# Kernel tuning notes

Measured on AMD Instinct MI355X. Metric: run time of the kernel, lower is better.

## Reference

```python
import jax, jax.numpy as jnp
import numpy as np

B, T, D, H = 8, 1024, 512, 8
HD = D // H
EPS = 1e-5


def setup_inputs() -> dict:
    key = jax.random.key(0)
    ks = jax.random.split(key, 16)
    s = 0.02
    return {
        "query": jax.random.normal(ks[0], (B, T, D), jnp.float32),
        "key": jax.random.normal(ks[1], (B, T, D), jnp.float32),
        "value": jax.random.normal(ks[2], (B, T, D), jnp.float32),
        "frac": jax.random.uniform(ks[3], (B, T), jnp.float32),
        "Wq": jax.random.normal(ks[4], (D, D), jnp.float32) * s,
        "bq": jnp.zeros((D,), jnp.float32),
        "Wk": jax.random.normal(ks[5], (D, D), jnp.float32) * s,
        "bk": jnp.zeros((D,), jnp.float32),
        "Wv": jax.random.normal(ks[6], (D, D), jnp.float32) * s,
        "bv": jnp.zeros((D,), jnp.float32),
        "Wo": jax.random.normal(ks[7], (D, D), jnp.float32) * s,
        "bo": jnp.zeros((D,), jnp.float32),
        # alpha params are zeros in torch init; use small randn so the bias path is non-degenerate
        "alpha_pos": jax.random.normal(ks[8], (H,), jnp.float32) * 0.1,
        "alpha_neg": jax.random.normal(ks[9], (H,), jnp.float32) * 0.1,
        "gamma": jnp.asarray(1.0, jnp.float32),
        "delta": jnp.asarray(0.2, jnp.float32),
        "add_frac_bias": 1,
    }


def _zscore_last(t):
    # torch.std uses unbiased estimator (ddof=1)
    m = t.mean(axis=-1, keepdims=True)
    s = jnp.std(t, axis=-1, keepdims=True, ddof=1)
    return (t - m) / (s + EPS)


def reference(query, key, value, frac, Wq, bq, Wk, bk, Wv, bv, Wo, bo,
              alpha_pos, alpha_neg, gamma, delta, add_frac_bias):
    b, t, d = query.shape
    h = alpha_pos.shape[0]
    hd = d // h
    scale = hd ** -0.5

    def proj(x, W, bias):
        return (x @ W + bias).reshape(b, t, h, hd).transpose(0, 2, 1, 3)  # [B,H,T,hd]

    Q = proj(query, Wq, bq)
    K = proj(key, Wk, bk)
    V = proj(value, Wv, bv)

    logits = jnp.einsum('bhqd,bhkd->bhqk', Q, K) * scale  # [B,H,T,T]

    fi = frac[:, :, None]          # [B,T,1]
    fj = frac[:, None, :]          # [B,1,T]
    Dm = (fj - fi) * (fi * fj)     # [B,T,T]
    D_pos = jax.nn.relu(Dm)
    D_neg = -jax.nn.relu(-Dm)
    stoich = (alpha_pos[None, :, None, None] * D_pos[:, None]
              + alpha_neg[None, :, None, None] * D_neg[:, None])  # [B,H,T,T]

    logits_z = _zscore_last(logits)
    if add_frac_bias:
        attn = gamma * logits_z + delta * _zscore_last(stoich)
    else:
        attn = gamma * logits_z

    probs = jax.nn.softmax(attn, axis=-1)
    out = jnp.einsum('bhqk,bhkd->bhqd', probs, V)  # [B,H,T,hd]
    out = out.transpose(0, 2, 1, 3).reshape(b, t, d)
    return out @ Wo + bo
```

## Files before the change

### kernel.cpp

```cpp
#include <hip/hip_runtime.h>
#include <hip/hip_bf16.h>

#define EPS 1e-5f
#define FLASH_SMEM 72704

typedef short bf16x8 __attribute__((ext_vector_type(8)));
typedef float f32x4 __attribute__((ext_vector_type(4)));

#define GL16(gp, lp) __builtin_amdgcn_global_load_lds( \
    (const __attribute__((address_space(1))) void*)(gp), \
    (__attribute__((address_space(3))) void*)(lp), 16, 0, 0)

__device__ __forceinline__ unsigned short f2bf(float f) {
  union { float f; unsigned u; } v; v.f = f;
  return (unsigned short)((v.u + 0x7FFFu + ((v.u >> 16) & 1u)) >> 16);
}
__device__ __forceinline__ float bf2f(unsigned short u) {
  return __uint_as_float(((unsigned)u) << 16);
}

__global__ void wtrans4_kernel(const float* __restrict__ W0, const float* __restrict__ W1,
                               const float* __restrict__ W2, const float* __restrict__ W3,
                               unsigned short* __restrict__ T0, unsigned short* __restrict__ T1,
                               unsigned short* __restrict__ T2, unsigned short* __restrict__ T3) {
  __shared__ float tile[32][33];
  int z = blockIdx.z;
  const float* W = z == 0 ? W0 : z == 1 ? W1 : z == 2 ? W2 : W3;
  unsigned short* Wt = z == 0 ? T0 : z == 1 ? T1 : z == 2 ? T2 : T3;
  float scale = (z == 0) ? 0.125f : 1.0f;
  int n0 = blockIdx.x * 32, k0 = blockIdx.y * 32;
  int c = threadIdx.x & 31, r0 = threadIdx.x >> 5;
  #pragma unroll
  for (int rr = 0; rr < 32; rr += 8)
    tile[r0 + rr][c] = W[(k0 + r0 + rr) * 512 + n0 + c];
  __syncthreads();
  #pragma unroll
  for (int rr = 0; rr < 32; rr += 8)
    Wt[(n0 + r0 + rr) * 512 + k0 + c] = f2bf(tile[c][r0 + rr] * scale);
}

__global__ void frac_stats_kernel(const float* __restrict__ frac,
                                  float* __restrict__ fstats) {
  int wid = (int)((blockIdx.x * blockDim.x + threadIdx.x) >> 6);
  int ln = threadIdx.x & 63;
  if (wid >= 8192) return;
  int b = wid >> 10, q = wid & 1023;
  const float* fr = frac + b * 1024;
  float fq = fr[q];
  float sp = 0.f, sn = 0.f, sp2 = 0.f, sn2 = 0.f;
  for (int i = ln; i < 1024; i += 64) {
    float f = fr[i];
    float dm = (f - fq) * (fq * f);
    float p = fmaxf(dm, 0.f), nn = fminf(dm, 0.f);
    sp += p; sn += nn; sp2 += p * p; sn2 += nn * nn;
  }
  #pragma unroll
  for (int m = 32; m; m >>= 1) {
    sp += __shfl_xor(sp, m); sn += __shfl_xor(sn, m);
    sp2 += __shfl_xor(sp2, m); sn2 += __shfl_xor(sn2, m);
  }
  if (ln == 0) {
    float4 o; o.x = sp; o.y = sn; o.z = sp2; o.w = sn2;
    *(float4*)(fstats + (size_t)wid * 4) = o;
  }
}

__global__ __launch_bounds__(256) void qkv_gemm_kernel(
    const float* __restrict__ Aq, const float* __restrict__ Ak, const float* __restrict__ Av,
    const unsigned short* __restrict__ WqT, const unsigned short* __restrict__ WkT,
    const unsigned short* __restrict__ WvT,
    const float* __restrict__ bq, const float* __restrict__ bk, const float* __restrict__ bv,
    unsigned short* __restrict__ Qh, unsigned short* __restrict__ Kh,
    unsigned short* __restrict__ Ktr, unsigned short* __restrict__ Vt) {
  __shared__ unsigned short Al[2][128 * 32];
  __shared__ unsigned short Bl[2][128 * 32];
  const int z = blockIdx.z;
  const float* A = z == 0 ? Aq : z == 1 ? Ak : Av;
  const unsigned short* Bt = z == 0 ? WqT : z == 1 ? WkT : WvT;
  const float* bias = z == 0 ? bq : z == 1 ? bk : bv;
  const float bscale = (z == 0) ? 0.125f : 1.0f;

  const int tid = threadIdx.x, ln = tid & 63, wv = tid >> 6;
  const int m0 = blockIdx.y * 128, n0 = blockIdx.x * 128;
  const int wr = wv >> 1, wc = wv & 1;
  const int arow = tid >> 1;
  const int agh = (tid & 1) * 2;

  auto stageB = [&](int kt, int buf) {
    int kb = kt * 32;
    #pragma unroll
    for (int u = 0; u < 2; ++u) {
      int n = tid + u * 256;
      int Lrow = n >> 2, kcs = n & 3;
      int kc = kcs ^ (Lrow & 3);
      GL16(Bt + (size_t)(n0 + Lrow) * 512 + kb + kc * 8, &Bl[buf][n * 8]);
    }
  };
  auto loadA = [&](int kt, float4* la) {
    const float* src = A + (size_t)(m0 + arow) * 512 + kt * 32 + agh * 8;
    la[0] = *(const float4*)(src);
    la[1] = *(const float4*)(src + 4);
    la[2] = *(const float4*)(src + 8);
    la[3] = *(const float4*)(src + 12);
  };
  auto writeA = [&](int buf, const float4* la) {
    #pragma unroll
    for (int G = 0; G < 2; ++G) {
      union { bf16x8 v; unsigned short u[8]; } pk;
      float4 a = la[2 * G], b2 = la[2 * G + 1];
      pk.u[0] = f2bf(a.x); pk.u[1] = f2bf(a.y); pk.u[2] = f2bf(a.z); pk.u[3] = f2bf(a.w);
      pk.u[4] = f2bf(b2.x); pk.u[5] = f2bf(b2.y); pk.u[6] = f2bf(b2.z); pk.u[7] = f2bf(b2.w);
      int dg = (agh + G) ^ (arow & 3);
      *(bf16x8*)(&Al[buf][arow * 32 + dg * 8]) = pk.v;
    }
  };

  f32x4 acc[4][4] = {};
  float4 la[4];
  loadA(0, la); writeA(0, la);
  stageB(0, 0);
  for (int kt = 0; kt < 16; ++kt) {
    __syncthreads();
    if (kt < 15) { loadA(kt + 1, la); stageB(kt + 1, (kt + 1) & 1); }
    const unsigned short* a_ = Al[kt & 1];
    const unsigned short* b_ = Bl[kt & 1];
    const int kc = ln >> 4;
    bf16x8 afr[4], bfr[4];
    #pragma unroll
    for (int m = 0; m < 4; ++m) {
      int r = wr * 64 + m * 16 + (ln & 15);
      afr[m] = *(const bf16x8*)(a_ + r * 32 + ((kc ^ (r & 3)) * 8));
    }
    #pragma unroll
    for (int n = 0; n < 4; ++n) {
      int r = wc * 64 + n * 16 + (ln & 15);
      bfr[n] = *(const bf16x8*)(b_ + r * 32 + ((kc ^ (r & 3)) * 8));
    }
    #pragma unroll
    for (int m = 0; m < 4; ++m)
      #pragma unroll
      for (int n = 0; n < 4; ++n)
        acc[m][n] = __builtin_amdgcn_mfma_f32_16x16x32_bf16(afr[m], bfr[n], acc[m][n], 0, 0, 0);
    if (kt < 15) writeA((kt + 1) & 1, la);
  }

  #pragma unroll
  for (int m = 0; m < 4; ++m) {
    #pragma unroll
    for (int n = 0; n < 4; ++n) {
      int gm0 = m0 + wr * 64 + m * 16 + (ln >> 4) * 4;
      int gn = n0 + wc * 64 + n * 16 + (ln & 15);
      float bvv = bias[gn] * bscale;
      int hh = gn >> 6, d = gn & 63;
      if (z < 2) {
        unsigned short* o = z == 0 ? Qh : Kh;
        #pragma unroll
        for (int i = 0; i < 4; ++i) {
          int gm = gm0 + i;
          int bb = gm >> 10, t = gm & 1023;
          o[(size_t)((bb * 8 + hh) * 1024 + t) * 64 + d] = f2bf(acc[m][n][i] + bvv);
        }
        if (z == 1) {
          int bb = gm0 >> 10, t = gm0 & 1023;
          ushort4 pk;
          pk.x = f2bf(acc[m][n][0] + bvv);
          pk.y = f2bf(acc[m][n][1] + bvv);
          pk.z = f2bf(acc[m][n][2] + bvv);
          pk.w = f2bf(acc[m][n][3] + bvv);
          *(ushort4*)(Ktr + (size_t)((bb * 8 + hh) * 64 + d) * 1024 + t) = pk;
        }
      } else {
        int bb = gm0 >> 10, t = gm0 & 1023;
        int k5 = t & 31;
        int pos = (t & ~31) + ((k5 >> 2) & 3) * 8 + ((k5 >> 4) & 1) * 4;
        ushort4 pk;
        pk.x = f2bf(acc[m][n][0] + bvv);
        pk.y = f2bf(acc[m][n][1] + bvv);
        pk.z = f2bf(acc[m][n][2] + bvv);
        pk.w = f2bf(acc[m][n][3] + bvv);
        *(ushort4*)(Vt + (size_t)((bb * 8 + hh) * 64 + d) * 1024 + pos) = pk;
      }
    }
  }
}

__global__ __launch_bounds__(256) void gemm_out_kernel(
    const unsigned short* __restrict__ A,
    const unsigned short* __restrict__ Bt,
    const float* __restrict__ bias,
    float* __restrict__ out) {
  __shared__ unsigned short Al[2][128 * 32];
  __shared__ unsigned short Bl[2][128 * 32];
  const int tid = threadIdx.x, ln = tid & 63, wv = tid >> 6;
  const int m0 = blockIdx.y * 128, n0 = blockIdx.x * 128;
  const int wr = wv >> 1, wc = wv & 1;

  auto stage = [&](int kt, int buf) {
    int kb = kt * 32;
    #pragma unroll
    for (int u = 0; u < 2; ++u) {
      int n = tid + u * 256;
      int Lrow = n >> 2, kcs = n & 3;
      int kc = kcs ^ (Lrow & 3);
      GL16(A + (size_t)(m0 + Lrow) * 512 + kb + kc * 8, &Al[buf][n * 8]);
      GL16(Bt + (size_t)(n0 + Lrow) * 512 + kb + kc * 8, &Bl[buf][n * 8]);
    }
  };

  f32x4 acc[4][4] = {};
  stage(0, 0);
  for (int kt = 0; kt < 16; ++kt) {
    __syncthreads();
    if (kt < 15) stage(kt + 1, (kt + 1) & 1);
    const unsigned short* a_ = Al[kt & 1];
    const unsigned short* b_ = Bl[kt & 1];
    const int kc = ln >> 4;
    bf16x8 afr[4], bfr[4];
    #pragma unroll
    for (int m = 0; m < 4; ++m) {
      int r = wr * 64 + m * 16 + (ln & 15);
      afr[m] = *(const bf16x8*)(a_ + r * 32 + ((kc ^ (r & 3)) * 8));
    }
    #pragma unroll
    for (int n = 0; n < 4; ++n) {
      int r = wc * 64 + n * 16 + (ln & 15);
      bfr[n] = *(const bf16x8*)(b_ + r * 32 + ((kc ^ (r & 3)) * 8));
    }
    #pragma unroll
    for (int m = 0; m < 4; ++m)
      #pragma unroll
      for (int n = 0; n < 4; ++n)
        acc[m][n] = __builtin_amdgcn_mfma_f32_16x16x32_bf16(afr[m], bfr[n], acc[m][n], 0, 0, 0);
  }
  #pragma unroll
  for (int m = 0; m < 4; ++m)
    #pragma unroll
    for (int n = 0; n < 4; ++n) {
      int gm0 = m0 + wr * 64 + m * 16 + (ln >> 4) * 4;
      int gn = n0 + wc * 64 + n * 16 + (ln & 15);
      float bvv = bias[gn];
      #pragma unroll
      for (int i = 0; i < 4; ++i)
        out[(size_t)(gm0 + i) * 512 + gn] = acc[m][n][i] + bvv;
    }
}

__global__ __launch_bounds__(256, 1) void gram_kernel(
    const unsigned short* __restrict__ Ktr,
    unsigned short* __restrict__ Mhi, unsigned short* __restrict__ Mlo,
    float* __restrict__ KsumG) {
  __shared__ float KsR[4][64];
  const int bh = blockIdx.x;
  const unsigned short* Kb = Ktr + (size_t)bh * 65536;
  const int tid = threadIdx.x, ln = tid & 63, w = tid >> 6;
  const int c = ln & 15, g = ln >> 4;

  f32x4 acc[4] = {};
  #pragma unroll 2
  for (int kk = 0; kk < 32; ++kk) {
    bf16x8 af = *(const bf16x8*)(Kb + (size_t)(w * 16 + c) * 1024 + kk * 32 + g * 8);
    #pragma unroll
    for (int jt = 0; jt < 4; ++jt) {
      bf16x8 bf = *(const bf16x8*)(Kb + (size_t)(jt * 16 + c) * 1024 + kk * 32 + g * 8);
      acc[jt] = __builtin_amdgcn_mfma_f32_16x16x32_bf16(af, bf, acc[jt], 0, 0, 0);
    }
  }
  #pragma unroll
  for (int jt = 0; jt < 4; ++jt)
    #pragma unroll
    for (int r = 0; r < 4; ++r) {
      float v = acc[jt][r];
      unsigned short hi = f2bf(v);
      unsigned short lo = f2bf(v - bf2f(hi));
      size_t idx = (size_t)bh * 4096 + (w * 16 + g * 4 + r) * 64 + jt * 16 + c;
      Mhi[idx] = hi;
      Mlo[idx] = lo;
    }

  int d = tid & 63, seg = tid >> 6;
  float s = 0.f;
  for (int u = 0; u < 32; ++u) {
    bf16x8 v8 = *(const bf16x8*)(Kb + (size_t)d * 1024 + seg * 256 + u * 8);
    #pragma unroll
    for (int e = 0; e < 8; ++e) s += bf2f((unsigned short)v8[e]);
  }
  KsR[seg][d] = s;
  __syncthreads();
  if (tid < 64)
    KsumG[bh * 64 + tid] = KsR[0][tid] + KsR[1][tid] + KsR[2][tid] + KsR[3][tid];
}

__global__ __launch_bounds__(256) void coef_kernel(
    const unsigned short* __restrict__ Qh,
    const unsigned short* __restrict__ Mhi, const unsigned short* __restrict__ Mlo,
    const float* __restrict__ KsumG,
    const float* __restrict__ frac, const float* __restrict__ fstats,
    const float* __restrict__ alpha_pos, const float* __restrict__ alpha_neg,
    const float* __restrict__ gamma_p, const float* __restrict__ delta_p,
    const int* __restrict__ afb_p,
    float4* __restrict__ rowcG, float* __restrict__ rowShG) {
  const int bh = blockIdx.y;
  const int b = bh >> 3, h = bh & 7;
  const int tid = threadIdx.x, ln = tid & 63, w = tid >> 6;
  const int c = ln & 15, g = ln >> 4;
  const int qrow0 = blockIdx.x * 64 + w * 16;

  const unsigned short* qa = Qh + (size_t)(bh * 1024 + qrow0 + c) * 64 + g * 8;
  bf16x8 aQ0 = *(const bf16x8*)(qa);
  bf16x8 aQ1 = *(const bf16x8*)(qa + 32);

  const unsigned short* Mh = Mhi + (size_t)bh * 4096;
  const unsigned short* Ml = Mlo + (size_t)bh * 4096;
  f32x4 acc[4] = {};
  #pragma unroll
  for (int jt = 0; jt < 4; ++jt) {
    const unsigned short* mrow = Mh + (jt * 16 + c) * 64 + g * 8;
    const unsigned short* lrow = Ml + (jt * 16 + c) * 64 + g * 8;
    bf16x8 bh0 = *(const bf16x8*)(mrow);
    bf16x8 bh1 = *(const bf16x8*)(mrow + 32);
    bf16x8 bl0 = *(const bf16x8*)(lrow);
    bf16x8 bl1 = *(const bf16x8*)(lrow + 32);
    acc[jt] = __builtin_amdgcn_mfma_f32_16x16x32_bf16(aQ0, bh0, acc[jt], 0, 0, 0);
    acc[jt] = __builtin_amdgcn_mfma_f32_16x16x32_bf16(aQ1, bh1, acc[jt], 0, 0, 0);
    acc[jt] = __builtin_amdgcn_mfma_f32_16x16x32_bf16(aQ0, bl0, acc[jt], 0, 0, 0);
    acc[jt] = __builtin_amdgcn_mfma_f32_16x16x32_bf16(aQ1, bl1, acc[jt], 0, 0, 0);
  }

  float ks[4];
  #pragma unroll
  for (int jt = 0; jt < 4; ++jt) ks[jt] = KsumG[bh * 64 + jt * 16 + c];
  float pl[4], p2[4];
  #pragma unroll
  for (int r = 0; r < 4; ++r) {
    const unsigned short* qd = Qh + (size_t)(bh * 1024 + qrow0 + g * 4 + r) * 64 + c;
    float l = 0.f, s2 = 0.f;
    #pragma unroll
    for (int jt = 0; jt < 4; ++jt) {
      float qv = bf2f(qd[jt * 16]);
      s2 += qv * acc[jt][r];
      l += qv * ks[jt];
    }
    pl[r] = l; p2[r] = s2;
  }
  #pragma unroll
  for (int m = 1; m < 16; m <<= 1)
    #pragma unroll
    for (int r = 0; r < 4; ++r) {
      pl[r] += __shfl_xor(pl[r], m);
      p2[r] += __shfl_xor(p2[r], m);
    }

  if (c == 0) {
    const float gmv = *gamma_p, dlv = *delta_p;
    const float ap = alpha_pos[h], an = alpha_neg[h];
    const int afb = *afb_p;
    const float L2E = 1.4426950408889634f;
    #pragma unroll
    for (int r = 0; r < 4; ++r) {
      int q = qrow0 + g * 4 + r;
      float sl = pl[r], sl2 = p2[r];
      float mul_ = sl * (1.f / 1024.f);
      float varl = fmaxf((sl2 - 1024.f * mul_ * mul_) * (1.f / 1023.f), 0.f);
      float cA = gmv / (sqrtf(varl) + EPS);
      float4 st = *(const float4*)(fstats + (size_t)(b * 1024 + q) * 4);
      float msum = ap * st.x + an * st.y;
      float msq = ap * ap * st.z + an * an * st.w;
      float mus = msum * (1.f / 1024.f);
      float vars = fmaxf((msq - 1024.f * mus * mus) * (1.f / 1023.f), 0.f);
      float cB = afb ? (dlv / (sqrtf(vars) + EPS)) : 0.f;
      float4 rc;
      rc.x = frac[b * 1024 + q];
      rc.y = cA * L2E;
      rc.z = cB * ap * L2E;
      rc.w = cB * an * L2E;
      rowcG[(size_t)bh * 1024 + q] = rc;
      rowShG[(size_t)bh * 1024 + q] = (cA * mul_ + cB * mus) * L2E;
    }
  }
}

__global__ __launch_bounds__(256, 2) void flash_kernel(
    const unsigned short* __restrict__ Qh,
    const unsigned short* __restrict__ Kh,
    const unsigned short* __restrict__ Vt,
    unsigned short* __restrict__ attnO,
    const float* __restrict__ frac,
    const float4* __restrict__ rowcG, const float* __restrict__ rowShG) {
  extern __shared__ char smem[];
  unsigned short* Kl = (unsigned short*)smem;
  unsigned short* Vl = (unsigned short*)(smem + 32768);
  float* fk = (float*)(smem + 65536);
  float4* rowcS = (float4*)(smem + 69632);
  float* rowShS = (float*)(smem + 71680);
  float* psumW = (float*)(smem + 72192);

  const int L = blockIdx.x;
  const int xcd = L & 7, s = L >> 3;
  const int bh = xcd + 8 * (s >> 3);
  const int t0 = (s & 7) * 128;
  const int b = bh >> 3, h = bh & 7;
  const int tid = threadIdx.x, ln = tid & 63, w = tid >> 6;
  const int c = ln & 15, g = ln >> 4;

  auto stageK = [&](int t, int buf) {
    #pragma unroll
    for (int u = 0; u < 4; ++u) {
      int n = tid + u * 256;
      int row = n >> 3, kc = (n & 7) ^ (row & 7);
      GL16(Kh + (size_t)(bh * 1024 + t * 128 + row) * 64 + kc * 8,
           Kl + buf * 8192 + n * 8);
    }
  };
  auto stageV = [&](int t, int buf) {
    #pragma unroll
    for (int u = 0; u < 4; ++u) {
      int n = tid + u * 256;
      int d = n >> 4, ch = n & 15;
      GL16(Vt + (size_t)(bh * 64 + d) * 1024 + t * 128 + (ch ^ (d & 15)) * 8,
           Vl + buf * 8192 + n * 8);
    }
  };

  stageK(0, 0);
  stageV(0, 0);
  GL16(frac + b * 1024 + tid * 4, fk + tid * 4);
  if (tid < 128) GL16(rowcG + (size_t)bh * 1024 + t0 + tid, rowcS + tid);
  if (tid < 32) GL16(rowShG + (size_t)bh * 1024 + t0 + tid * 4, rowShS + tid * 4);

  bf16x8 qf[2][2];
  #pragma unroll
  for (int qh = 0; qh < 2; ++qh) {
    const unsigned short* qrow =
        Qh + (size_t)(bh * 1024 + t0 + w * 32 + qh * 16 + c) * 64 + g * 8;
    qf[qh][0] = *(const bf16x8*)(qrow);
    qf[qh][1] = *(const bf16x8*)(qrow + 32);
  }
  __syncthreads();

  const float4 rc0 = rowcS[w * 32 + c], rc1 = rowcS[w * 32 + 16 + c];
  const float sh0 = rowShS[w * 32 + c], sh1 = rowShS[w * 32 + 16 + c];

  f32x4 acc[2][4] = {};
  float ps0a = 0.f, ps0b = 0.f, ps1a = 0.f, ps1b = 0.f;

  for (int t = 0; t < 8; ++t) {
    if (t) __syncthreads();
    if (t < 7) { stageK(t + 1, (t + 1) & 1); stageV(t + 1, (t + 1) & 1); }
    const unsigned short* kb_ = Kl + (t & 1) * 8192;
    const unsigned short* vb_ = Vl + (t & 1) * 8192;

    f32x4 S[8][2];
    #pragma unroll
    for (int kg = 0; kg < 8; ++kg) {
      int krow = kg * 16 + c;
      bf16x8 kf0 = *(const bf16x8*)(kb_ + krow * 64 + ((g ^ (krow & 7)) * 8));
      bf16x8 kf1 = *(const bf16x8*)(kb_ + krow * 64 + (((g + 4) ^ (krow & 7)) * 8));
      #pragma unroll
      for (int qh = 0; qh < 2; ++qh) {
        f32x4 a = {0.f, 0.f, 0.f, 0.f};
        a = __builtin_amdgcn_mfma_f32_16x16x32_bf16(kf0, qf[qh][0], a, 0, 0, 0);
        a = __builtin_amdgcn_mfma_f32_16x16x32_bf16(kf1, qf[qh][1], a, 0, 0, 0);
        S[kg][qh] = a;
      }
    }

    #pragma unroll
    for (int kg = 0; kg < 8; ++kg) {
      float4 f4 = *(const float4*)(&fk[t * 128 + kg * 16 + g * 4]);
      #pragma unroll
      for (int r = 0; r < 4; ++r) {
        float f = (r == 0) ? f4.x : (r == 1) ? f4.y : (r == 2) ? f4.z : f4.w;
        {
          float dd = f - rc0.x, x = f * rc0.x * dd;
          float sel = (dd >= 0.f) ? rc0.z : rc0.w;
          float e = __builtin_amdgcn_exp2f(fmaf(rc0.y, S[kg][0][r], fmaf(x, sel, -sh0)));
          if (kg & 1) ps0a += e; else ps0b += e;
          S[kg][0][r] = e;
        }
        {
          float dd = f - rc1.x, x = f * rc1.x * dd;
          float sel = (dd >= 0.f) ? rc1.z : rc1.w;
          float e = __builtin_amdgcn_exp2f(fmaf(rc1.y, S[kg][1][r], fmaf(x, sel, -sh1)));
          if (kg & 1) ps1a += e; else ps1b += e;
          S[kg][1][r] = e;
        }
      }
    }

    __builtin_amdgcn_s_setprio(1);
    #pragma unroll
    for (int ks = 0; ks < 4; ++ks) {
      union AW { unsigned u[4]; bf16x8 v; } aw0, aw1;
      #pragma unroll
      for (int m = 0; m < 4; ++m) {
        int kg2 = 2 * ks + (m >> 1), rr = (m & 1) * 2;
        unsigned a0 = __float_as_uint(S[kg2][0][rr]), a1 = __float_as_uint(S[kg2][0][rr + 1]);
        aw0.u[m] = ((a1 + 0x8000u) & 0xFFFF0000u) | ((a0 + 0x8000u) >> 16);
        unsigned b0 = __float_as_uint(S[kg2][1][rr]), b1 = __float_as_uint(S[kg2][1][rr + 1]);
        aw1.u[m] = ((b1 + 0x8000u) & 0xFFFF0000u) | ((b0 + 0x8000u) >> 16);
      }
      #pragma unroll
      for (int db = 0; db < 4; ++db) {
        int d = db * 16 + c;
        bf16x8 bv = *(const bf16x8*)(vb_ + d * 128 + (((ks * 4 + g) ^ c) * 8));
        acc[0][db] = __builtin_amdgcn_mfma_f32_16x16x32_bf16(aw0.v, bv, acc[0][db], 0, 0, 0);
        acc[1][db] = __builtin_amdgcn_mfma_f32_16x16x32_bf16(aw1.v, bv, acc[1][db], 0, 0, 0);
      }
    }
    __builtin_amdgcn_s_setprio(0);
  }

  float ps0 = ps0a + ps0b, ps1 = ps1a + ps1b;
  ps0 += __shfl_xor(ps0, 16); ps0 += __shfl_xor(ps0, 32);
  ps1 += __shfl_xor(ps1, 16); ps1 += __shfl_xor(ps1, 32);
  if (g == 0) { psumW[w * 32 + c] = ps0; psumW[w * 32 + 16 + c] = ps1; }

  #pragma unroll
  for (int qh = 0; qh < 2; ++qh)
    #pragma unroll
    for (int r = 0; r < 4; ++r) {
      float rcp = 1.f / psumW[w * 32 + qh * 16 + g * 4 + r];
      int qg = t0 + w * 32 + qh * 16 + g * 4 + r;
      unsigned short* orow = attnO + (size_t)(b * 1024 + qg) * 512 + h * 64 + c;
      #pragma unroll
      for (int db = 0; db < 4; ++db)
        orow[db * 16] = f2bf(acc[qh][db][r] * rcp);
    }
}

extern "C" void kernel_launch(void* const* d_in, const int* in_sizes, int n_in,
                              void* d_out, int out_size, void* d_ws, size_t ws_size,
                              hipStream_t stream) {
  const float* q = (const float*)d_in[0];
  const float* k = (const float*)d_in[1];
  const float* v = (const float*)d_in[2];
  const float* frac = (const float*)d_in[3];
  const float* Wq = (const float*)d_in[4];
  const float* bq = (const float*)d_in[5];
  const float* Wk = (const float*)d_in[6];
  const float* bk = (const float*)d_in[7];
  const float* Wv = (const float*)d_in[8];
  const float* bv = (const float*)d_in[9];
  const float* Wo = (const float*)d_in[10];
  const float* bo = (const float*)d_in[11];
  const float* ap = (const float*)d_in[12];
  const float* an = (const float*)d_in[13];
  const float* gm = (const float*)d_in[14];
  const float* dl = (const float*)d_in[15];
  const int* afb = (const int*)d_in[16];

  char* ws = (char*)d_ws;
  unsigned short* wqT = (unsigned short*)(ws + 0);
  unsigned short* wkT = (unsigned short*)(ws + 524288);
  unsigned short* wvT = (unsigned short*)(ws + 1048576);
  unsigned short* woT = (unsigned short*)(ws + 1572864);
  unsigned short* Qh = (unsigned short*)(ws + 2097152);
  unsigned short* Kh = (unsigned short*)(ws + 10485760);
  unsigned short* Ktr = (unsigned short*)(ws + 18874368);
  unsigned short* Vt = (unsigned short*)(ws + 27262976);
  unsigned short* aO = (unsigned short*)(ws + 35651584);
  float* fst = (float*)(ws + 44040192);
  unsigned short* Mhi = (unsigned short*)(ws + 44171264);
  unsigned short* Mlo = (unsigned short*)(ws + 44695552);
  float* KsumG = (float*)(ws + 45219840);
  float4* rowcG = (float4*)(ws + 45236224);
  float* rowShG = (float*)(ws + 46284800);

  hipFuncSetAttribute((const void*)flash_kernel,
                      hipFuncAttributeMaxDynamicSharedMemorySize, FLASH_SMEM);

  wtrans4_kernel<<<dim3(16, 16, 4), 256, 0, stream>>>(Wq, Wk, Wv, Wo, wqT, wkT, wvT, woT);
  frac_stats_kernel<<<2048, 256, 0, stream>>>(frac, fst);
  qkv_gemm_kernel<<<dim3(4, 64, 3), 256, 0, stream>>>(q, k, v, wqT, wkT, wvT,
                                                      bq, bk, bv, Qh, Kh, Ktr, Vt);
  gram_kernel<<<64, 256, 0, stream>>>(Ktr, Mhi, Mlo, KsumG);
  coef_kernel<<<dim3(16, 64), 256, 0, stream>>>(Qh, Mhi, Mlo, KsumG, frac, fst,
                                                ap, an, gm, dl, afb, rowcG, rowShG);
  flash_kernel<<<512, 256, FLASH_SMEM, stream>>>(Qh, Kh, Vt, aO, frac, rowcG, rowShG);
  gemm_out_kernel<<<dim3(4, 64), 256, 0, stream>>>(aO, woT, bo, (float*)d_out);
}
```

Baseline: 137.4 us.

## Stage QKV epilogue through LDS for coalesced stores and remap blocks per XCD

```diff
diff --git a/kernel.cpp b/kernel.cpp
--- a/kernel.cpp
+++ b/kernel.cpp
@@ -74,15 +74,21 @@
     unsigned short* __restrict__ Ktr, unsigned short* __restrict__ Vt) {
   __shared__ unsigned short Al[2][128 * 32];
   __shared__ unsigned short Bl[2][128 * 32];
-  const int z = blockIdx.z;
+  const int L = blockIdx.x;
+  const int xcd = L & 7, sl = L >> 3;
+  const int xb = sl & 3;
+  const int P = (sl >> 2) * 8 + xcd;
+  const int yb = P & 63, z = P >> 6;
+
   const float* A = z == 0 ? Aq : z == 1 ? Ak : Av;
   const unsigned short* Bt = z == 0 ? WqT : z == 1 ? WkT : WvT;
   const float* bias = z == 0 ? bq : z == 1 ? bk : bv;
   const float bscale = (z == 0) ? 0.125f : 1.0f;
 
   const int tid = threadIdx.x, ln = tid & 63, wv = tid >> 6;
-  const int m0 = blockIdx.y * 128, n0 = blockIdx.x * 128;
+  const int m0 = yb * 128, n0 = xb * 128;
   const int wr = wv >> 1, wc = wv & 1;
+  const int c = ln & 15, g = ln >> 4;
   const int arow = tid >> 1;
   const int agh = (tid & 1) * 2;
 
@@ -128,12 +134,12 @@
     bf16x8 afr[4], bfr[4];
     #pragma unroll
     for (int m = 0; m < 4; ++m) {
-      int r = wr * 64 + m * 16 + (ln & 15);
+      int r = wr * 64 + m * 16 + c;
       afr[m] = *(const bf16x8*)(a_ + r * 32 + ((kc ^ (r & 3)) * 8));
     }
     #pragma unroll
     for (int n = 0; n < 4; ++n) {
-      int r = wc * 64 + n * 16 + (ln & 15);
+      int r = wc * 64 + n * 16 + c;
       bfr[n] = *(const bf16x8*)(b_ + r * 32 + ((kc ^ (r & 3)) * 8));
     }
     #pragma unroll
@@ -144,41 +150,71 @@
     if (kt < 15) writeA((kt + 1) & 1, la);
   }
 
-  #pragma unroll
-  for (int m = 0; m < 4; ++m) {
-    #pragma unroll
-    for (int n = 0; n < 4; ++n) {
-      int gm0 = m0 + wr * 64 + m * 16 + (ln >> 4) * 4;
-      int gn = n0 + wc * 64 + n * 16 + (ln & 15);
-      float bvv = bias[gn] * bscale;
-      int hh = gn >> 6, d = gn & 63;
-      if (z < 2) {
-        unsigned short* o = z == 0 ? Qh : Kh;
+  float bv4[4];
+  #pragma unroll
+  for (int n = 0; n < 4; ++n) bv4[n] = bias[n0 + wc * 64 + n * 16 + c] * bscale;
+
+  const int bb = yb >> 3;
+  const int hh = xb * 2 + wc;
+  const int t_base = (m0 & 1023) + wr * 64;
+  unsigned short* W = (wv < 2) ? &Al[wv][0] : &Bl[wv - 2][0];
+  const size_t headBase = (size_t)(bb * 8 + hh);
+
+  __syncthreads();
+
+  if (z < 2) {
+    #pragma unroll
+    for (int m = 0; m < 4; ++m)
+      #pragma unroll
+      for (int n = 0; n < 4; ++n)
         #pragma unroll
         for (int i = 0; i < 4; ++i) {
-          int gm = gm0 + i;
-          int bb = gm >> 10, t = gm & 1023;
-          o[(size_t)((bb * 8 + hh) * 1024 + t) * 64 + d] = f2bf(acc[m][n][i] + bvv);
+          int lt = m * 16 + g * 4 + i;
+          int lc = n * 16 + c;
+          W[lt * 64 + (((lc >> 3) ^ (lt & 7)) * 8) + (lc & 7)] = f2bf(acc[m][n][i] + bv4[n]);
         }
-        if (z == 1) {
-          int bb = gm0 >> 10, t = gm0 & 1023;
-          ushort4 pk;
-          pk.x = f2bf(acc[m][n][0] + bvv);
-          pk.y = f2bf(acc[m][n][1] + bvv);
-          pk.z = f2bf(acc[m][n][2] + bvv);
-          pk.w = f2bf(acc[m][n][3] + bvv);
-          *(ushort4*)(Ktr + (size_t)((bb * 8 + hh) * 64 + d) * 1024 + t) = pk;
+    __syncthreads();
+    unsigned short* o = (z == 0 ? Qh : Kh) + (headBase * 1024 + t_base) * 64;
+    #pragma unroll
+    for (int j = 0; j < 8; ++j) {
+      int lt = j * 8 + (ln >> 3), ch = ln & 7;
+      bf16x8 vv = *(const bf16x8*)(W + lt * 64 + ((ch ^ (lt & 7)) * 8));
+      *(bf16x8*)(o + j * 512 + ln * 8) = vv;
+    }
+  }
+  if (z >= 1) {
+    __syncthreads();
+    #pragma unroll
+    for (int m = 0; m < 4; ++m)
+      #pragma unroll
+      for (int n = 0; n < 4; ++n)
+        #pragma unroll
+        for (int i = 0; i < 4; ++i) {
+          int lt = m * 16 + g * 4 + i;
+          int lc = n * 16 + c;
+          W[lc * 64 + (((lt >> 3) ^ (lc & 7)) * 8) + (lt & 7)] = f2bf(acc[m][n][i] + bv4[n]);
         }
-      } else {
-        int bb = gm0 >> 10, t = gm0 & 1023;
-        int k5 = t & 31;
-        int pos = (t & ~31) + ((k5 >> 2) & 3) * 8 + ((k5 >> 4) & 1) * 4;
-        ushort4 pk;
-        pk.x = f2bf(acc[m][n][0] + bvv);
-        pk.y = f2bf(acc[m][n][1] + bvv);
-        pk.z = f2bf(acc[m][n][2] + bvv);
-        pk.w = f2bf(acc[m][n][3] + bvv);
-        *(ushort4*)(Vt + (size_t)((bb * 8 + hh) * 64 + d) * 1024 + pos) = pk;
+    __syncthreads();
+    if (z == 1) {
+      unsigned short* o = Ktr + headBase * 65536 + t_base;
+      #pragma unroll
+      for (int j = 0; j < 8; ++j) {
+        int d = j * 8 + (ln >> 3), ch = ln & 7;
+        bf16x8 vv = *(const bf16x8*)(W + d * 64 + ((ch ^ (d & 7)) * 8));
+        *(bf16x8*)(o + (size_t)d * 1024 + ch * 8) = vv;
+      }
+    } else {
+      unsigned short* o = Vt + headBase * 65536 + t_base;
+      #pragma unroll
+      for (int j = 0; j < 8; ++j) {
+        int d = j * 8 + (ln >> 3), c8 = ln & 7;
+        int t1 = (c8 >> 2) * 32 + (c8 & 3) * 4;
+        int t2 = t1 + 16;
+        ushort4 lo = *(const ushort4*)(W + d * 64 + (((t1 >> 3) ^ (d & 7)) * 8) + (t1 & 7));
+        ushort4 hi = *(const ushort4*)(W + d * 64 + (((t2 >> 3) ^ (d & 7)) * 8) + (t2 & 7));
+        union { ushort4 s[2]; bf16x8 v; } pk;
+        pk.s[0] = lo; pk.s[1] = hi;
+        *(bf16x8*)(o + (size_t)d * 1024 + c8 * 8) = pk.v;
       }
     }
   }
@@ -191,8 +227,11 @@
     float* __restrict__ out) {
   __shared__ unsigned short Al[2][128 * 32];
   __shared__ unsigned short Bl[2][128 * 32];
+  const int L = blockIdx.x;
+  const int xcd = L & 7, sl = L >> 3;
+  const int xb = sl & 3, yb = (sl >> 2) * 8 + xcd;
   const int tid = threadIdx.x, ln = tid & 63, wv = tid >> 6;
-  const int m0 = blockIdx.y * 128, n0 = blockIdx.x * 128;
+  const int m0 = yb * 128, n0 = xb * 128;
   const int wr = wv >> 1, wc = wv & 1;
 
   auto stage = [&](int kt, int buf) {
@@ -571,11 +610,11 @@
 
   wtrans4_kernel<<<dim3(16, 16, 4), 256, 0, stream>>>(Wq, Wk, Wv, Wo, wqT, wkT, wvT, woT);
   frac_stats_kernel<<<2048, 256, 0, stream>>>(frac, fst);
-  qkv_gemm_kernel<<<dim3(4, 64, 3), 256, 0, stream>>>(q, k, v, wqT, wkT, wvT,
-                                                      bq, bk, bv, Qh, Kh, Ktr, Vt);
+  qkv_gemm_kernel<<<768, 256, 0, stream>>>(q, k, v, wqT, wkT, wvT,
+                                           bq, bk, bv, Qh, Kh, Ktr, Vt);
   gram_kernel<<<64, 256, 0, stream>>>(Ktr, Mhi, Mlo, KsumG);
   coef_kernel<<<dim3(16, 64), 256, 0, stream>>>(Qh, Mhi, Mlo, KsumG, frac, fst,
                                                 ap, an, gm, dl, afb, rowcG, rowShG);
   flash_kernel<<<512, 256, FLASH_SMEM, stream>>>(Qh, Kh, Vt, aO, frac, rowcG, rowShG);
-  gemm_out_kernel<<<dim3(4, 64), 256, 0, stream>>>(aO, woT, bo, (float*)d_out);
-}
+  gemm_out_kernel<<<256, 256, 0, stream>>>(aO, woT, bo, (float*)d_out);
+}
```

Measured after the change: 137.6 us. No clear change (+0.1%).
